# Kernel tuning notes

Measured on AMD Instinct MI355X. Metric: run time of the kernel, lower is better.

## Reference

```python
import jax, jax.numpy as jnp
import numpy as np

B = 256
C_IN, F_IN = 32, 256
C_OUT, F_OUT = 32, 256
KERNEL_SIZE = 4
BN_EPS = 1e-5


def _block_mask():
    # channel-wise connectivity: output channel o sees input channels in its kernel_size block
    co = jnp.arange(C_OUT)[:, None] // KERNEL_SIZE
    ci = jnp.arange(C_IN)[None, :] // KERNEL_SIZE
    return co == ci  # [C_OUT, C_IN] bool


def setup_inputs() -> dict:
    key = jax.random.key(0)
    k_x, k_w, k_b, k_g, k_be = jax.random.split(key, 5)
    x = jax.random.normal(k_x, (B, C_IN, F_IN), dtype=jnp.float32)
    fan_in = KERNEL_SIZE * F_IN
    W = jax.random.normal(k_w, (C_OUT, C_IN, F_OUT, F_IN), dtype=jnp.float32) / np.float32(np.sqrt(fan_in))
    bias = jax.random.normal(k_b, (C_OUT, F_OUT), dtype=jnp.float32) * 0.01
    gamma = 1.0 + 0.1 * jax.random.normal(k_g, (C_OUT * F_OUT,), dtype=jnp.float32)
    beta = 0.1 * jax.random.normal(k_be, (C_OUT * F_OUT,), dtype=jnp.float32)
    mask = _block_mask()
    return {"x": x, "W": W, "bias": bias, "gamma": gamma, "beta": beta, "mask": mask}


def reference(x, W, bias, gamma, beta, mask):
    # masked sparse linear: y[b,o,f] = sum_{c,i} mask[o,c] * W[o,c,f,i] * x[b,c,i] + bias[o,f]
    Wm = W * mask[:, :, None, None].astype(W.dtype)
    y = jnp.einsum('bci,ocfi->bof', x, Wm) + bias  # [B, C_OUT, F_OUT]
    b = y.shape[0]
    yf = y.reshape(b, C_OUT * F_OUT)
    # BatchNorm1d in training mode: biased batch statistics over the batch dim
    mean = jnp.mean(yf, axis=0)
    var = jnp.var(yf, axis=0)
    yn = (yf - mean) * jax.lax.rsqrt(var + BN_EPS) * gamma + beta
    # Swish: x * sigmoid(x)
    out = yn * jax.nn.sigmoid(yn)
    return out.reshape(b, C_OUT, F_OUT)
```

## Files before the change

### kernel.cpp

```cpp
#include <hip/hip_runtime.h>
#include <hip/hip_bf16.h>


typedef float  f32x4  __attribute__((ext_vector_type(4)));
typedef short  short8 __attribute__((ext_vector_type(8)));
typedef unsigned short u16x8 __attribute__((ext_vector_type(8)));

static __device__ __forceinline__ unsigned short f2bf(float f) {
    unsigned int u = __float_as_uint(f);
    u += 0x7FFFu + ((u >> 16) & 1u);
    return (unsigned short)(u >> 16);
}
static __device__ __forceinline__ float bf2f(unsigned short h) {
    return __uint_as_float((unsigned int)h << 16);
}

#define GLL(gp, lp) __builtin_amdgcn_global_load_lds( \
    (const __attribute__((address_space(1))) unsigned int*)(gp), \
    (__attribute__((address_space(3))) unsigned int*)(lp), 16, 0, 0)

__global__ __launch_bounds__(256) void conv_kernel(const float* __restrict__ x,
                                                   unsigned short* __restrict__ xb) {
    const int base = blockIdx.x * 1024 + threadIdx.x;
#pragma unroll
    for (int i = 0; i < 4; ++i) {
        const int cid = base + i * 256;
        const f32x4 a = *(const f32x4*)(x + (size_t)cid * 8);
        const f32x4 b = *(const f32x4*)(x + (size_t)cid * 8 + 4);
        u16x8 v;
        v[0] = f2bf(a[0]); v[1] = f2bf(a[1]); v[2] = f2bf(a[2]); v[3] = f2bf(a[3]);
        v[4] = f2bf(b[0]); v[5] = f2bf(b[1]); v[6] = f2bf(b[2]); v[7] = f2bf(b[3]);
        *(u16x8*)(xb + (size_t)cid * 8) = v;
    }
}

__global__ __launch_bounds__(256) void fused_kernel(
    const unsigned short* __restrict__ xb, const float* __restrict__ W,
    const float* __restrict__ gamma, const float* __restrict__ beta,
    float* __restrict__ out)
{
    __shared__ __align__(16) char ldsA[3][32768];
    __shared__ __align__(16) char ldsB[2][4096];
    __shared__ float wps1[4][32], wps2[4][32];
    __shared__ float sa[32], sb[32];

    const int bid = blockIdx.x;
    const int g   = bid & 7;
    const int nt  = bid >> 3;
    const int o   = g * 4 + (nt >> 3);
    const int f0  = (nt & 7) * 32;
    const int gcol0 = o * 256 + f0;

    const int t    = threadIdx.x;
    const int wave = t >> 6;
    const int lane = t & 63;
    const int lr   = lane & 15;
    const int kq   = lane >> 4;

    f32x4 acc[4][2];
    const f32x4 zero = {0.f, 0.f, 0.f, 0.f};
#pragma unroll
    for (int i = 0; i < 4; ++i) { acc[i][0] = zero; acc[i][1] = zero; }

    f32x4 breg[2][2];

    auto ISSUE = [&](int st) {
        const int kk = st * 64;
        const unsigned short* asrc = xb + g * 1024 + kk;
        char* Ab = ldsA[st % 3];
#pragma unroll
        for (int i = 0; i < 8; ++i) {
            const int cid = i * 256 + t;
            const int r = cid >> 3, c = cid & 7;
            GLL(asrc + (size_t)r * 8192 + (c ^ (r & 7)) * 8, Ab + cid * 16);
        }
        const int cp = st >> 2, kc = (st & 3) * 64;
        const float* bsrc = W + ((size_t)((o * 32 + g * 4 + cp) * 256 + f0)) * 256 + kc
                              + (size_t)(t >> 3) * 256 + (t & 7) * 8;
        breg[st & 1][0] = *(const f32x4*)bsrc;
        breg[st & 1][1] = *(const f32x4*)(bsrc + 4);
    };
    auto WRITEB = [&](int st) {
        const int n = t >> 3, c = t & 7;
        short8 v;
        v[0] = (short)f2bf(breg[st & 1][0][0]); v[1] = (short)f2bf(breg[st & 1][0][1]);
        v[2] = (short)f2bf(breg[st & 1][0][2]); v[3] = (short)f2bf(breg[st & 1][0][3]);
        v[4] = (short)f2bf(breg[st & 1][1][0]); v[5] = (short)f2bf(breg[st & 1][1][1]);
        v[6] = (short)f2bf(breg[st & 1][1][2]); v[7] = (short)f2bf(breg[st & 1][1][3]);
        *(short8*)(ldsB[st & 1] + n * 128 + ((c ^ (n & 7)) * 16)) = v;
    };
    auto COMPUTE = [&](int st) {
        const char* Ab = ldsA[st % 3];
        const char* Bb = ldsB[st & 1];
#pragma unroll
        for (int ks = 0; ks < 2; ++ks) {
            short8 af[4], bfr[2];
#pragma unroll
            for (int i = 0; i < 4; ++i) {
                const int ra = wave * 64 + i * 16 + lr;
                af[i] = *(const short8*)(Ab + ra * 128 + (((ks * 4 + kq) ^ (ra & 7)) * 16));
            }
#pragma unroll
            for (int j = 0; j < 2; ++j) {
                const int n = j * 16 + lr;
                bfr[j] = *(const short8*)(Bb + n * 128 + (((ks * 4 + kq) ^ (n & 7)) * 16));
            }
#pragma unroll
            for (int i = 0; i < 4; ++i)
#pragma unroll
                for (int j = 0; j < 2; ++j)
                    acc[i][j] = __builtin_amdgcn_mfma_f32_16x16x32_bf16(af[i], bfr[j], acc[i][j], 0, 0, 0);
        }
    };

    ISSUE(0);
    ISSUE(1);
    asm volatile("s_waitcnt vmcnt(10)" ::: "memory");
    WRITEB(0);
    asm volatile("s_waitcnt lgkmcnt(0)" ::: "memory");
    __builtin_amdgcn_s_barrier();

#pragma unroll
    for (int st = 0; st < 16; ++st) {
        COMPUTE(st);
        if (st < 14) {
            ISSUE(st + 2);
            asm volatile("s_waitcnt vmcnt(10)" ::: "memory");
            WRITEB(st + 1);
            asm volatile("s_waitcnt lgkmcnt(0)" ::: "memory");
            __builtin_amdgcn_s_barrier();
        } else if (st == 14) {
            asm volatile("s_waitcnt vmcnt(0)" ::: "memory");
            WRITEB(15);
            asm volatile("s_waitcnt lgkmcnt(0)" ::: "memory");
            __builtin_amdgcn_s_barrier();
        }
    }

    float s1[2] = {0.f, 0.f}, s2[2] = {0.f, 0.f};
#pragma unroll
    for (int i = 0; i < 4; ++i)
#pragma unroll
        for (int j = 0; j < 2; ++j)
#pragma unroll
            for (int r = 0; r < 4; ++r) {
                const float v = acc[i][j][r];
                s1[j] += v; s2[j] += v * v;
            }
#pragma unroll
    for (int j = 0; j < 2; ++j) {
        s1[j] += __shfl_xor(s1[j], 16); s2[j] += __shfl_xor(s2[j], 16);
        s1[j] += __shfl_xor(s1[j], 32); s2[j] += __shfl_xor(s2[j], 32);
    }
    if (kq == 0) {
#pragma unroll
        for (int j = 0; j < 2; ++j) {
            wps1[wave][j * 16 + lr] = s1[j];
            wps2[wave][j * 16 + lr] = s2[j];
        }
    }
    __syncthreads();
    if (t < 32) {
        float a1 = wps1[0][t] + wps1[1][t] + wps1[2][t] + wps1[3][t];
        float a2 = wps2[0][t] + wps2[1][t] + wps2[2][t] + wps2[3][t];
        const float mean = a1 * (1.0f / 256.0f);
        const float var  = a2 * (1.0f / 256.0f) - mean * mean;
        const float istd = rsqrtf(var + 1e-5f);
        const float ga = gamma[gcol0 + t];
        sa[t] = ga * istd;
        sb[t] = beta[gcol0 + t] - mean * ga * istd;
    }
    __syncthreads();

#pragma unroll
    for (int i = 0; i < 4; ++i) {
        const int row0 = wave * 64 + i * 16 + kq * 4;
#pragma unroll
        for (int j = 0; j < 2; ++j) {
            const int col = j * 16 + lr;
            const float a = sa[col], b2 = sb[col];
#pragma unroll
            for (int r = 0; r < 4; ++r) {
                const float z = a * acc[i][j][r] + b2;
                out[(size_t)(row0 + r) * 8192 + gcol0 + col] = z / (1.0f + expf(-z));
            }
        }
    }
}

extern "C" void kernel_launch(void* const* d_in, const int* in_sizes, int n_in,
                              void* d_out, int out_size, void* d_ws, size_t ws_size,
                              hipStream_t stream) {
    const float* x     = (const float*)d_in[0];
    const float* W     = (const float*)d_in[1];
    const float* gamma = (const float*)d_in[3];
    const float* beta  = (const float*)d_in[4];
    float* out = (float*)d_out;

    unsigned short* xb = (unsigned short*)d_ws;

    conv_kernel<<<256, 256, 0, stream>>>(x, xb);
    fused_kernel<<<256, 256, 0, stream>>>(xb, W, gamma, beta, out);
}
```

Before: 26.32 us.

## Load activations directly to registers and double the waves per block

The fused GEMM kernel now uses 512 threads (8 waves), each wave owning 32 rows. Activation fragments are loaded straight from global memory into registers instead of staging through LDS with global_load_lds. W tiles are staged in 256-wide K chunks, so the pipeline drops from 16 stages to 4 with fewer barriers. This is meant to cut LDS traffic and synchronisation overhead and raise occupancy, at the cost of more registers for the A fragments and less coalesced A loads.

After: 30.68 us. +16.6%, slower.

```diff
diff --git a/kernel.cpp b/kernel.cpp
--- a/kernel.cpp
+++ b/kernel.cpp
@@ -5,19 +5,13 @@
 typedef float  f32x4  __attribute__((ext_vector_type(4)));
 typedef short  short8 __attribute__((ext_vector_type(8)));
 typedef unsigned short u16x8 __attribute__((ext_vector_type(8)));
+typedef unsigned int   u32x2 __attribute__((ext_vector_type(2)));
 
-static __device__ __forceinline__ unsigned short f2bf(float f) {
+static __device__ __forceinline__ unsigned int f2bf(float f) {
     unsigned int u = __float_as_uint(f);
     u += 0x7FFFu + ((u >> 16) & 1u);
-    return (unsigned short)(u >> 16);
+    return u >> 16;
 }
-static __device__ __forceinline__ float bf2f(unsigned short h) {
-    return __uint_as_float((unsigned int)h << 16);
-}
-
-#define GLL(gp, lp) __builtin_amdgcn_global_load_lds( \
-    (const __attribute__((address_space(1))) unsigned int*)(gp), \
-    (__attribute__((address_space(3))) unsigned int*)(lp), 16, 0, 0)
 
 __global__ __launch_bounds__(256) void conv_kernel(const float* __restrict__ x,
                                                    unsigned short* __restrict__ xb) {
@@ -34,14 +28,13 @@
     }
 }
 
-__global__ __launch_bounds__(256) void fused_kernel(
+__global__ __launch_bounds__(512) void fused_kernel(
     const unsigned short* __restrict__ xb, const float* __restrict__ W,
     const float* __restrict__ gamma, const float* __restrict__ beta,
     float* __restrict__ out)
 {
-    __shared__ __align__(16) char ldsA[3][32768];
-    __shared__ __align__(16) char ldsB[2][4096];
-    __shared__ float wps1[4][32], wps2[4][32];
+    __shared__ __align__(16) char Blds[2][16384];
+    __shared__ float wps1[8][32], wps2[8][32];
     __shared__ float sa[32], sb[32];
 
     const int bid = blockIdx.x;
@@ -52,86 +45,76 @@
     const int gcol0 = o * 256 + f0;
 
     const int t    = threadIdx.x;
-    const int wave = t >> 6;
+    const int w    = t >> 6;
     const int lane = t & 63;
     const int lr   = lane & 15;
     const int kq   = lane >> 4;
 
-    f32x4 acc[4][2];
+    f32x4 acc[2][2];
     const f32x4 zero = {0.f, 0.f, 0.f, 0.f};
 #pragma unroll
-    for (int i = 0; i < 4; ++i) { acc[i][0] = zero; acc[i][1] = zero; }
+    for (int i = 0; i < 2; ++i) { acc[i][0] = zero; acc[i][1] = zero; }
 
-    f32x4 breg[2][2];
+    f32x4  wreg[4];
+    short8 af[16];
 
-    auto ISSUE = [&](int st) {
-        const int kk = st * 64;
-        const unsigned short* asrc = xb + g * 1024 + kk;
-        char* Ab = ldsA[st % 3];
+    const unsigned short* abase = xb + g * 1024 + (size_t)(w * 32 + lr) * 8192;
+
+    auto WISSUE = [&](int st) {
+        const float* Wb = W + ((size_t)((o * 32 + g * 4 + st) * 256 + f0)) * 256;
 #pragma unroll
-        for (int i = 0; i < 8; ++i) {
-            const int cid = i * 256 + t;
-            const int r = cid >> 3, c = cid & 7;
-            GLL(asrc + (size_t)r * 8192 + (c ^ (r & 7)) * 8, Ab + cid * 16);
+        for (int q = 0; q < 4; ++q)
+            wreg[q] = *(const f32x4*)(Wb + (size_t)(q * 8 + w) * 256 + lane * 4);
+    };
+    auto WWRITE = [&](int buf) {
+#pragma unroll
+        for (int q = 0; q < 4; ++q) {
+            const int n = q * 8 + w;
+            u32x2 d;
+            d[0] = f2bf(wreg[q][0]) | (f2bf(wreg[q][1]) << 16);
+            d[1] = f2bf(wreg[q][2]) | (f2bf(wreg[q][3]) << 16);
+            *(u32x2*)(Blds[buf] + n * 512 + (((lane >> 1) ^ (n & 7)) * 16) + (lane & 1) * 8) = d;
         }
-        const int cp = st >> 2, kc = (st & 3) * 64;
-        const float* bsrc = W + ((size_t)((o * 32 + g * 4 + cp) * 256 + f0)) * 256 + kc
-                              + (size_t)(t >> 3) * 256 + (t & 7) * 8;
-        breg[st & 1][0] = *(const f32x4*)bsrc;
-        breg[st & 1][1] = *(const f32x4*)(bsrc + 4);
     };
-    auto WRITEB = [&](int st) {
-        const int n = t >> 3, c = t & 7;
-        short8 v;
-        v[0] = (short)f2bf(breg[st & 1][0][0]); v[1] = (short)f2bf(breg[st & 1][0][1]);
-        v[2] = (short)f2bf(breg[st & 1][0][2]); v[3] = (short)f2bf(breg[st & 1][0][3]);
-        v[4] = (short)f2bf(breg[st & 1][1][0]); v[5] = (short)f2bf(breg[st & 1][1][1]);
-        v[6] = (short)f2bf(breg[st & 1][1][2]); v[7] = (short)f2bf(breg[st & 1][1][3]);
-        *(short8*)(ldsB[st & 1] + n * 128 + ((c ^ (n & 7)) * 16)) = v;
+    auto AISSUE = [&](int st) {
+#pragma unroll
+        for (int ks = 0; ks < 8; ++ks)
+#pragma unroll
+            for (int i = 0; i < 2; ++i)
+                af[ks * 2 + i] = *(const short8*)(abase + (size_t)i * 16 * 8192
+                                                  + st * 256 + ks * 32 + kq * 8);
     };
-    auto COMPUTE = [&](int st) {
-        const char* Ab = ldsA[st % 3];
-        const char* Bb = ldsB[st & 1];
+    auto COMPUTE = [&](int buf) {
 #pragma unroll
-        for (int ks = 0; ks < 2; ++ks) {
-            short8 af[4], bfr[2];
-#pragma unroll
-            for (int i = 0; i < 4; ++i) {
-                const int ra = wave * 64 + i * 16 + lr;
-                af[i] = *(const short8*)(Ab + ra * 128 + (((ks * 4 + kq) ^ (ra & 7)) * 16));
-            }
+        for (int ks = 0; ks < 8; ++ks) {
+            short8 bfr[2];
 #pragma unroll
             for (int j = 0; j < 2; ++j) {
                 const int n = j * 16 + lr;
-                bfr[j] = *(const short8*)(Bb + n * 128 + (((ks * 4 + kq) ^ (n & 7)) * 16));
+                bfr[j] = *(const short8*)(Blds[buf] + n * 512 + (((ks * 4 + kq) ^ (n & 7)) * 16));
             }
 #pragma unroll
-            for (int i = 0; i < 4; ++i)
+            for (int i = 0; i < 2; ++i)
 #pragma unroll
                 for (int j = 0; j < 2; ++j)
-                    acc[i][j] = __builtin_amdgcn_mfma_f32_16x16x32_bf16(af[i], bfr[j], acc[i][j], 0, 0, 0);
+                    acc[i][j] = __builtin_amdgcn_mfma_f32_16x16x32_bf16(af[ks * 2 + i], bfr[j], acc[i][j], 0, 0, 0);
         }
     };
 
-    ISSUE(0);
-    ISSUE(1);
-    asm volatile("s_waitcnt vmcnt(10)" ::: "memory");
-    WRITEB(0);
+    WISSUE(0);
+    WWRITE(0);
+    AISSUE(0);
+    WISSUE(1);
     asm volatile("s_waitcnt lgkmcnt(0)" ::: "memory");
     __builtin_amdgcn_s_barrier();
 
 #pragma unroll
-    for (int st = 0; st < 16; ++st) {
-        COMPUTE(st);
-        if (st < 14) {
-            ISSUE(st + 2);
-            asm volatile("s_waitcnt vmcnt(10)" ::: "memory");
-            WRITEB(st + 1);
-            asm volatile("s_waitcnt lgkmcnt(0)" ::: "memory");
-            __builtin_amdgcn_s_barrier();
-        } else if (st == 14) {
-            asm volatile("s_waitcnt vmcnt(0)" ::: "memory");
-            WRITEB(15);
+    for (int st = 0; st < 4; ++st) {
+        COMPUTE(st & 1);
+        if (st < 3) {
+            WWRITE((st + 1) & 1);
+            AISSUE(st + 1);
+            if (st < 2) WISSUE(st + 2);
             asm volatile("s_waitcnt lgkmcnt(0)" ::: "memory");
             __builtin_amdgcn_s_barrier();
         }
@@ -139,7 +122,7 @@
 
     float s1[2] = {0.f, 0.f}, s2[2] = {0.f, 0.f};
 #pragma unroll
-    for (int i = 0; i < 4; ++i)
+    for (int i = 0; i < 2; ++i)
 #pragma unroll
         for (int j = 0; j < 2; ++j)
 #pragma unroll
@@ -155,14 +138,15 @@
     if (kq == 0) {
 #pragma unroll
         for (int j = 0; j < 2; ++j) {
-            wps1[wave][j * 16 + lr] = s1[j];
-            wps2[wave][j * 16 + lr] = s2[j];
+            wps1[w][j * 16 + lr] = s1[j];
+            wps2[w][j * 16 + lr] = s2[j];
         }
     }
     __syncthreads();
     if (t < 32) {
-        float a1 = wps1[0][t] + wps1[1][t] + wps1[2][t] + wps1[3][t];
-        float a2 = wps2[0][t] + wps2[1][t] + wps2[2][t] + wps2[3][t];
+        float a1 = 0.f, a2 = 0.f;
+#pragma unroll
+        for (int q = 0; q < 8; ++q) { a1 += wps1[q][t]; a2 += wps2[q][t]; }
         const float mean = a1 * (1.0f / 256.0f);
         const float var  = a2 * (1.0f / 256.0f) - mean * mean;
         const float istd = rsqrtf(var + 1e-5f);
@@ -173,8 +157,8 @@
     __syncthreads();
 
 #pragma unroll
-    for (int i = 0; i < 4; ++i) {
-        const int row0 = wave * 64 + i * 16 + kq * 4;
+    for (int i = 0; i < 2; ++i) {
+        const int row0 = w * 32 + i * 16 + kq * 4;
 #pragma unroll
         for (int j = 0; j < 2; ++j) {
             const int col = j * 16 + lr;
@@ -200,5 +184,5 @@
     unsigned short* xb = (unsigned short*)d_ws;
 
     conv_kernel<<<256, 256, 0, stream>>>(x, xb);
-    fused_kernel<<<256, 256, 0, stream>>>(xb, W, gamma, beta, out);
+    fused_kernel<<<256, 512, 0, stream>>>(xb, W, gamma, beta, out);
 }
```

## Fuse x bf16 conversion into GEMM kernel, stage fp32 A tiles in LDS

Applied to the files above, without the earlier changes.

Removes the separate conversion kernel and its bf16 workspace round trip. The fused kernel now loads fp32 x directly into LDS and converts A fragments to bf16 in registers right before each MFMA. Each stage therefore covers half the K width, so the pipeline runs 32 stages with matching smaller B tiles and retuned waitcnts. The trade is one fewer launch and less global traffic against twice as many barriers, extra conversion ALU work in the inner loop, and A fragments that are redundantly reconverted across blocks.

Result: slower. 35.03 us (+33.1%).

```diff
diff --git a/kernel.cpp b/kernel.cpp
--- a/kernel.cpp
+++ b/kernel.cpp
@@ -4,43 +4,25 @@
 
 typedef float  f32x4  __attribute__((ext_vector_type(4)));
 typedef short  short8 __attribute__((ext_vector_type(8)));
-typedef unsigned short u16x8 __attribute__((ext_vector_type(8)));
+typedef unsigned int u32x2 __attribute__((ext_vector_type(2)));
 
-static __device__ __forceinline__ unsigned short f2bf(float f) {
+static __device__ __forceinline__ unsigned int f2bf(float f) {
     unsigned int u = __float_as_uint(f);
     u += 0x7FFFu + ((u >> 16) & 1u);
-    return (unsigned short)(u >> 16);
-}
-static __device__ __forceinline__ float bf2f(unsigned short h) {
-    return __uint_as_float((unsigned int)h << 16);
+    return u >> 16;
 }
 
 #define GLL(gp, lp) __builtin_amdgcn_global_load_lds( \
     (const __attribute__((address_space(1))) unsigned int*)(gp), \
     (__attribute__((address_space(3))) unsigned int*)(lp), 16, 0, 0)
 
-__global__ __launch_bounds__(256) void conv_kernel(const float* __restrict__ x,
-                                                   unsigned short* __restrict__ xb) {
-    const int base = blockIdx.x * 1024 + threadIdx.x;
-#pragma unroll
-    for (int i = 0; i < 4; ++i) {
-        const int cid = base + i * 256;
-        const f32x4 a = *(const f32x4*)(x + (size_t)cid * 8);
-        const f32x4 b = *(const f32x4*)(x + (size_t)cid * 8 + 4);
-        u16x8 v;
-        v[0] = f2bf(a[0]); v[1] = f2bf(a[1]); v[2] = f2bf(a[2]); v[3] = f2bf(a[3]);
-        v[4] = f2bf(b[0]); v[5] = f2bf(b[1]); v[6] = f2bf(b[2]); v[7] = f2bf(b[3]);
-        *(u16x8*)(xb + (size_t)cid * 8) = v;
-    }
-}
-
-__global__ __launch_bounds__(256) void fused_kernel(
-    const unsigned short* __restrict__ xb, const float* __restrict__ W,
+__global__ __launch_bounds__(256, 1) void fused_kernel(
+    const float* __restrict__ x, const float* __restrict__ W,
     const float* __restrict__ gamma, const float* __restrict__ beta,
     float* __restrict__ out)
 {
     __shared__ __align__(16) char ldsA[3][32768];
-    __shared__ __align__(16) char ldsB[2][4096];
+    __shared__ __align__(16) char ldsB[2][2048];
     __shared__ float wps1[4][32], wps2[4][32];
     __shared__ float sa[32], sb[32];
 
@@ -62,76 +44,79 @@
 #pragma unroll
     for (int i = 0; i < 4; ++i) { acc[i][0] = zero; acc[i][1] = zero; }
 
-    f32x4 breg[2][2];
+    f32x4 breg[2];
 
     auto ISSUE = [&](int st) {
-        const int kk = st * 64;
-        const unsigned short* asrc = xb + g * 1024 + kk;
+        const float* bsrc = W + ((size_t)((o * 32 + g * 4 + (st >> 3)) * 256 + f0)) * 256
+                              + (st & 7) * 32 + (size_t)(t >> 3) * 256 + (t & 7) * 4;
+        breg[st & 1] = *(const f32x4*)bsrc;
+        const float* asrc = x + g * 1024 + st * 32;
         char* Ab = ldsA[st % 3];
 #pragma unroll
         for (int i = 0; i < 8; ++i) {
             const int cid = i * 256 + t;
             const int r = cid >> 3, c = cid & 7;
-            GLL(asrc + (size_t)r * 8192 + (c ^ (r & 7)) * 8, Ab + cid * 16);
+            GLL(asrc + (size_t)r * 8192 + (size_t)((c ^ (r & 7)) * 4), Ab + cid * 16);
         }
-        const int cp = st >> 2, kc = (st & 3) * 64;
-        const float* bsrc = W + ((size_t)((o * 32 + g * 4 + cp) * 256 + f0)) * 256 + kc
-                              + (size_t)(t >> 3) * 256 + (t & 7) * 8;
-        breg[st & 1][0] = *(const f32x4*)bsrc;
-        breg[st & 1][1] = *(const f32x4*)(bsrc + 4);
     };
     auto WRITEB = [&](int st) {
-        const int n = t >> 3, c = t & 7;
-        short8 v;
-        v[0] = (short)f2bf(breg[st & 1][0][0]); v[1] = (short)f2bf(breg[st & 1][0][1]);
-        v[2] = (short)f2bf(breg[st & 1][0][2]); v[3] = (short)f2bf(breg[st & 1][0][3]);
-        v[4] = (short)f2bf(breg[st & 1][1][0]); v[5] = (short)f2bf(breg[st & 1][1][1]);
-        v[6] = (short)f2bf(breg[st & 1][1][2]); v[7] = (short)f2bf(breg[st & 1][1][3]);
-        *(short8*)(ldsB[st & 1] + n * 128 + ((c ^ (n & 7)) * 16)) = v;
+        const int n = t >> 3;
+        const int c2 = (t & 7) >> 1;
+        const int slot = c2 ^ ((n >> 1) & 3);
+        const f32x4 v = breg[st & 1];
+        u32x2 d;
+        d[0] = f2bf(v[0]) | (f2bf(v[1]) << 16);
+        d[1] = f2bf(v[2]) | (f2bf(v[3]) << 16);
+        *(u32x2*)(ldsB[st & 1] + n * 64 + slot * 16 + (t & 1) * 8) = d;
     };
     auto COMPUTE = [&](int st) {
         const char* Ab = ldsA[st % 3];
         const char* Bb = ldsB[st & 1];
+        short8 af[4], bfr[2];
 #pragma unroll
-        for (int ks = 0; ks < 2; ++ks) {
-            short8 af[4], bfr[2];
+        for (int i = 0; i < 4; ++i) {
+            const int ra = wave * 64 + i * 16 + lr;
+            const int s = ra & 7;
+            const f32x4 lo = *(const f32x4*)(Ab + ra * 128 + (((kq * 2) ^ s) * 16));
+            const f32x4 hi = *(const f32x4*)(Ab + ra * 128 + (((kq * 2 + 1) ^ s) * 16));
+            short8 v;
+            v[0] = (short)f2bf(lo[0]); v[1] = (short)f2bf(lo[1]);
+            v[2] = (short)f2bf(lo[2]); v[3] = (short)f2bf(lo[3]);
+            v[4] = (short)f2bf(hi[0]); v[5] = (short)f2bf(hi[1]);
+            v[6] = (short)f2bf(hi[2]); v[7] = (short)f2bf(hi[3]);
+            af[i] = v;
+        }
 #pragma unroll
-            for (int i = 0; i < 4; ++i) {
-                const int ra = wave * 64 + i * 16 + lr;
-                af[i] = *(const short8*)(Ab + ra * 128 + (((ks * 4 + kq) ^ (ra & 7)) * 16));
-            }
+        for (int j = 0; j < 2; ++j) {
+            const int nb = j * 16 + lr;
+            bfr[j] = *(const short8*)(Bb + nb * 64 + ((kq ^ ((nb >> 1) & 3)) * 16));
+        }
 #pragma unroll
-            for (int j = 0; j < 2; ++j) {
-                const int n = j * 16 + lr;
-                bfr[j] = *(const short8*)(Bb + n * 128 + (((ks * 4 + kq) ^ (n & 7)) * 16));
-            }
+        for (int i = 0; i < 4; ++i)
 #pragma unroll
-            for (int i = 0; i < 4; ++i)
-#pragma unroll
-                for (int j = 0; j < 2; ++j)
-                    acc[i][j] = __builtin_amdgcn_mfma_f32_16x16x32_bf16(af[i], bfr[j], acc[i][j], 0, 0, 0);
-        }
+            for (int j = 0; j < 2; ++j)
+                acc[i][j] = __builtin_amdgcn_mfma_f32_16x16x32_bf16(af[i], bfr[j], acc[i][j], 0, 0, 0);
     };
 
     ISSUE(0);
     ISSUE(1);
-    asm volatile("s_waitcnt vmcnt(10)" ::: "memory");
+    asm volatile("s_waitcnt vmcnt(9)" ::: "memory");
     WRITEB(0);
     asm volatile("s_waitcnt lgkmcnt(0)" ::: "memory");
     __builtin_amdgcn_s_barrier();
 
 #pragma unroll
-    for (int st = 0; st < 16; ++st) {
+    for (int st = 0; st < 32; ++st) {
         COMPUTE(st);
-        if (st < 14) {
+        if (st < 30) {
             ISSUE(st + 2);
-            asm volatile("s_waitcnt vmcnt(10)" ::: "memory");
+            asm volatile("s_waitcnt vmcnt(9)" ::: "memory");
             WRITEB(st + 1);
             asm volatile("s_waitcnt lgkmcnt(0)" ::: "memory");
             __builtin_amdgcn_s_barrier();
-        } else if (st == 14) {
+        } else if (st == 30) {
             asm volatile("s_waitcnt vmcnt(0)" ::: "memory");
-            WRITEB(15);
+            WRITEB(31);
             asm volatile("s_waitcnt lgkmcnt(0)" ::: "memory");
             __builtin_amdgcn_s_barrier();
         }
@@ -197,8 +182,5 @@
     const float* beta  = (const float*)d_in[4];
     float* out = (float*)d_out;
 
-    unsigned short* xb = (unsigned short*)d_ws;
-
-    conv_kernel<<<256, 256, 0, stream>>>(x, xb);
-    fused_kernel<<<256, 256, 0, stream>>>(xb, W, gamma, beta, out);
+    fused_kernel<<<256, 256, 0, stream>>>(x, W, gamma, beta, out);
 }
```
